# Performance work log

Measured on AMD Instinct MI355X. Metric: run time of the kernel, lower is better.

## Reference

```python
import jax, jax.numpy as jnp
import numpy as np

N_NODES = 100000


def setup_inputs() -> dict:
    key = jax.random.key(0)
    k1, k2, k3, k4 = jax.random.split(key, 4)
    N, E, D_IN, D_OUT = N_NODES, 3200000, 256, 256
    feature = jax.random.normal(k1, (N, D_IN), dtype=jnp.float32)
    edge_src = jax.random.randint(k2, (E,), 0, N, dtype=jnp.int32)
    edge_dst = jax.random.randint(k3, (E,), 0, N, dtype=jnp.int32)
    W = jax.random.normal(k4, (D_IN, D_OUT), dtype=jnp.float32) * (1.0 / np.sqrt(D_IN))
    b = jnp.zeros((D_OUT,), dtype=jnp.float32)
    return {"feature": feature, "edge_src": edge_src, "edge_dst": edge_dst, "W": W, "b": b}


def reference(feature, edge_src, edge_dst, W, b):
    # update_all(copy_src('h','m'), sum('m','h')): for each node i,
    # h_i = sum over edges (j->i) of feature[j]  -- scatter-add by destination.
    msgs = feature[edge_src]                                   # [E, D_in] (gather)
    agg = jax.ops.segment_sum(msgs, edge_dst, num_segments=N_NODES)  # [N, D_in]
    # apply_nodes: Linear + activation (relu)
    h = jnp.dot(agg, W) + b                                    # [N, D_out]
    return jax.nn.relu(h)
```

## Files before the change

### kernel.cpp

```cpp
#include <hip/hip_runtime.h>

#define D 256
#define GSIZE 16
#define TN 16
#define CSHIFT 8
#define CBIN 256
#define NCMAX 512
#define CAPC 9216
#define NB_P 256
#define TILESHIFT 12
#define NKEY 8192

using bf16x8 = __attribute__((ext_vector_type(8))) short;
using f32x4  = __attribute__((ext_vector_type(4))) float;

__device__ inline float bf_lo(unsigned int u) {
    return __builtin_bit_cast(float, u << 16);
}
__device__ inline float bf_hi(unsigned int u) {
    return __builtin_bit_cast(float, u & 0xffff0000u);
}
__device__ inline unsigned short f2bf(float f) {
    unsigned int x = __builtin_bit_cast(unsigned int, f);
    unsigned int r = (x + 0x7fffu + ((x >> 16) & 1u)) >> 16;
    return (unsigned short)r;
}

__global__ __launch_bounds__(256) void part_kernel(
    const int* __restrict__ src, const int* __restrict__ dst,
    int* __restrict__ gcntC, int* __restrict__ csrA,
    const float* __restrict__ feature, unsigned short* __restrict__ fbf, long n8,
    const float* __restrict__ W, unsigned short* __restrict__ Wt,
    int E, int NC, int chunk, int nConvF)
{
    __shared__ int h[NCMAX];
    const int b = blockIdx.x, t = threadIdx.x;

    if (b < NB_P) {
        for (int i = t; i < NC; i += 256) h[i] = 0;
        __syncthreads();
        const int beg = b * chunk;
        const int end = min(beg + chunk, E);
        for (int i = beg + t; i < end; i += 256)
            atomicAdd(&h[dst[i] >> CSHIFT], 1);
        __syncthreads();
        for (int i = t; i < NC; i += 256) {
            int c = h[i];
            h[i] = c ? atomicAdd(&gcntC[i], c) : 0;
        }
        __syncthreads();
        for (int i = beg + t; i < end; i += 256) {
            int d = dst[i];
            int c = d >> CSHIFT;
            int r = atomicAdd(&h[c], 1);
            if (r < CAPC)
                csrA[(size_t)c * CAPC + r] = (src[i] << CSHIFT) | (d & (CBIN - 1));
        }
        return;
    }
    if (b < NB_P + nConvF) {
        long i = (long)(b - NB_P) * 256 + t;
        if (i < n8) {
            const float4* p = reinterpret_cast<const float4*>(feature + i * 8);
            float4 v0 = p[0], v1 = p[1];
            uint4 r;
            r.x = (unsigned int)f2bf(v0.x) | ((unsigned int)f2bf(v0.y) << 16);
            r.y = (unsigned int)f2bf(v0.z) | ((unsigned int)f2bf(v0.w) << 16);
            r.z = (unsigned int)f2bf(v1.x) | ((unsigned int)f2bf(v1.y) << 16);
            r.w = (unsigned int)f2bf(v1.z) | ((unsigned int)f2bf(v1.w) << 16);
            *reinterpret_cast<uint4*>(fbf + i * 8) = r;
        }
        return;
    }
    int i = (b - NB_P - nConvF) * 256 + t;
    if (i < D * D / 4) {
        int n  = i >> 6;
        int k0 = (i & 63) * 4;
        float a  = W[(size_t)(k0 + 0) * D + n];
        float bb = W[(size_t)(k0 + 1) * D + n];
        float c  = W[(size_t)(k0 + 2) * D + n];
        float d  = W[(size_t)(k0 + 3) * D + n];
        uint2 r;
        r.x = (unsigned int)f2bf(a) | ((unsigned int)f2bf(bb) << 16);
        r.y = (unsigned int)f2bf(c) | ((unsigned int)f2bf(d) << 16);
        *reinterpret_cast<uint2*>(Wt + (size_t)n * D + k0) = r;
    }
}

__global__ __launch_bounds__(256) void regroup_kernel(
    const int* __restrict__ csrA, const int* __restrict__ gcntC,
    int* __restrict__ csrB, int* __restrict__ nodeBeg, int* __restrict__ nodeCnt,
    int N)
{
    __shared__ int h[NKEY];
    __shared__ int sorted[CAPC];
    __shared__ int psum[256];
    __shared__ int nBegL[CBIN], nCntL[CBIN];
    const int c = blockIdx.x, t = threadIdx.x;
    const size_t rbeg = (size_t)c * CAPC;
    const int cnt = min(gcntC[c], CAPC);

    for (int i = t; i < NKEY; i += 256) h[i] = 0;
    __syncthreads();
    for (int i = t; i < cnt; i += 256) {
        int p = csrA[rbeg + i];
        int key = ((p & (CBIN - 1)) << 5) | ((p >> CSHIFT) >> TILESHIFT);
        atomicAdd(&h[key], 1);
    }
    __syncthreads();
    int local = 0;
#pragma unroll
    for (int j = 0; j < 32; ++j) local += h[(t << 5) + j];
    psum[t] = local;
    nCntL[t] = local;
    __syncthreads();
    for (int off = 1; off < 256; off <<= 1) {
        int v = (t >= off) ? psum[t - off] : 0;
        __syncthreads();
        if (t >= off) psum[t] += v;
        __syncthreads();
    }
    int run = (t == 0) ? 0 : psum[t - 1];
    nBegL[t] = run;
#pragma unroll
    for (int j = 0; j < 32; ++j) {
        int idx = (t << 5) + j;
        int cc = h[idx];
        h[idx] = run;
        run += cc;
    }
    __syncthreads();
    for (int i = t; i < cnt; i += 256) {
        int p = csrA[rbeg + i];
        int key = ((p & (CBIN - 1)) << 5) | ((p >> CSHIFT) >> TILESHIFT);
        int r = atomicAdd(&h[key], 1);
        sorted[r] = p >> CSHIFT;
    }
    __syncthreads();
    for (int i = t; i < cnt; i += 256)
        csrB[rbeg + i] = sorted[i];
    {
        int node = (c << CSHIFT) + t;
        if (node < N) {
            nodeBeg[node] = (int)(rbeg + nBegL[t]);
            nodeCnt[node] = nCntL[t];
        }
    }
}

__global__ __launch_bounds__(256) void agg_gemm_kernel(
    const unsigned short* __restrict__ fbf,
    const int* __restrict__ csrB,
    const int* __restrict__ nodeBeg,
    const int* __restrict__ nodeCnt,
    const unsigned short* __restrict__ Wt,
    const float* __restrict__ bias,
    float* __restrict__ out, int N)
{
    __shared__ int nBeg[TN], nCnt[TN];
    __shared__ unsigned short A[TN][D + 8];

    const int blk  = blockIdx.x;
    const int t    = threadIdx.x;
    const int wave = t >> 6;
    const int lane = t & 63;
    const int sub  = lane & 31;
    const int half = lane >> 5;
    const int node0 = blk * TN;
    const size_t colOff = (size_t)(sub << 3);

    if (t < TN) {
        int node = node0 + t;
        nBeg[t] = (node < N) ? nodeBeg[node] : 0;
        nCnt[t] = (node < N) ? nodeCnt[node] : 0;
    }
    __syncthreads();

    for (int ni = 0; ni < 4; ++ni) {
        const int l = (wave << 2) + ni;
        const int node = node0 + l;
        float a0 = 0.f, a1 = 0.f, a2 = 0.f, a3 = 0.f;
        float a4 = 0.f, a5 = 0.f, a6 = 0.f, a7 = 0.f;
        if (node < N) {
            const int b0 = nBeg[l];
            const int c0 = nCnt[l];
            int j = 0;
            for (; j + 3 < c0; j += 4) {
                int s0 = csrB[b0 + j + half];
                int s1 = csrB[b0 + j + 2 + half];
                uint4 v0 = *reinterpret_cast<const uint4*>(fbf + ((size_t)s0 << 8) + colOff);
                uint4 v1 = *reinterpret_cast<const uint4*>(fbf + ((size_t)s1 << 8) + colOff);
                a0 += bf_lo(v0.x); a1 += bf_hi(v0.x); a2 += bf_lo(v0.y); a3 += bf_hi(v0.y);
                a4 += bf_lo(v0.z); a5 += bf_hi(v0.z); a6 += bf_lo(v0.w); a7 += bf_hi(v0.w);
                a0 += bf_lo(v1.x); a1 += bf_hi(v1.x); a2 += bf_lo(v1.y); a3 += bf_hi(v1.y);
                a4 += bf_lo(v1.z); a5 += bf_hi(v1.z); a6 += bf_lo(v1.w); a7 += bf_hi(v1.w);
            }
            if (j + 1 < c0) {
                int s0 = csrB[b0 + j + half];
                uint4 v0 = *reinterpret_cast<const uint4*>(fbf + ((size_t)s0 << 8) + colOff);
                a0 += bf_lo(v0.x); a1 += bf_hi(v0.x); a2 += bf_lo(v0.y); a3 += bf_hi(v0.y);
                a4 += bf_lo(v0.z); a5 += bf_hi(v0.z); a6 += bf_lo(v0.w); a7 += bf_hi(v0.w);
                j += 2;
            }
            if (j < c0 && half == 0) {
                int s0 = csrB[b0 + j];
                uint4 v0 = *reinterpret_cast<const uint4*>(fbf + ((size_t)s0 << 8) + colOff);
                a0 += bf_lo(v0.x); a1 += bf_hi(v0.x); a2 += bf_lo(v0.y); a3 += bf_hi(v0.y);
                a4 += bf_lo(v0.z); a5 += bf_hi(v0.z); a6 += bf_lo(v0.w); a7 += bf_hi(v0.w);
            }
        }
        a0 += __shfl_xor(a0, 32); a1 += __shfl_xor(a1, 32);
        a2 += __shfl_xor(a2, 32); a3 += __shfl_xor(a3, 32);
        a4 += __shfl_xor(a4, 32); a5 += __shfl_xor(a5, 32);
        a6 += __shfl_xor(a6, 32); a7 += __shfl_xor(a7, 32);
        if (half == 0) {
            uint4 r;
            r.x = (unsigned int)f2bf(a0) | ((unsigned int)f2bf(a1) << 16);
            r.y = (unsigned int)f2bf(a2) | ((unsigned int)f2bf(a3) << 16);
            r.z = (unsigned int)f2bf(a4) | ((unsigned int)f2bf(a5) << 16);
            r.w = (unsigned int)f2bf(a6) | ((unsigned int)f2bf(a7) << 16);
            *reinterpret_cast<uint4*>(&A[l][sub << 3]) = r;
        }
    }
    __syncthreads();

    const int lr = lane & 15;
    const int lg = lane >> 4;

    bf16x8 afr[8];
#pragma unroll
    for (int ks = 0; ks < 8; ++ks)
        afr[ks] = *reinterpret_cast<const bf16x8*>(&A[lr][ks * 32 + lg * 8]);

#pragma unroll
    for (int c = 0; c < 4; ++c) {
        const int ct = (wave << 2) + c;
        f32x4 acc = {0.f, 0.f, 0.f, 0.f};
        const unsigned short* bp = Wt + (size_t)(ct * 16 + lr) * D + lg * 8;
#pragma unroll
        for (int ks = 0; ks < 8; ++ks) {
            bf16x8 bfr = *reinterpret_cast<const bf16x8*>(bp + ks * 32);
            acc = __builtin_amdgcn_mfma_f32_16x16x32_bf16(afr[ks], bfr, acc, 0, 0, 0);
        }
        const float bv = bias[ct * 16 + lr];
#pragma unroll
        for (int jj = 0; jj < 4; ++jj) {
            int row = node0 + lg * 4 + jj;
            if (row < N) {
                float v = acc[jj] + bv;
                out[(size_t)row * D + ct * 16 + lr] = v > 0.f ? v : 0.f;
            }
        }
    }
}

__global__ __launch_bounds__(256) void scatter_kernel(
    const float* __restrict__ feature, const int* __restrict__ src,
    const int* __restrict__ dst, float* __restrict__ agg, int E)
{
    int edge = blockIdx.x * (blockDim.x >> 6) + (threadIdx.x >> 6);
    int lane = threadIdx.x & 63;
    if (edge >= E) return;
    int s = src[edge];
    int d = dst[edge];
    const float4 v = *reinterpret_cast<const float4*>(feature + (size_t)s * D + lane * 4);
    float* o = agg + (size_t)d * D + lane * 4;
    atomicAdd(o + 0, v.x);
    atomicAdd(o + 1, v.y);
    atomicAdd(o + 2, v.z);
    atomicAdd(o + 3, v.w);
}

#define BM 32
__global__ __launch_bounds__(256) void linear_relu_kernel(
    float* __restrict__ h, const float* __restrict__ W,
    const float* __restrict__ b, int n_nodes)
{
    __shared__ float sA[BM][D];
    const int node0 = blockIdx.x * BM;
    const int t = threadIdx.x;
    for (int m = 0; m < BM; ++m) {
        int nd = node0 + m;
        sA[m][t] = (nd < n_nodes) ? h[(size_t)nd * D + t] : 0.0f;
    }
    __syncthreads();
    float acc[BM];
#pragma unroll
    for (int m = 0; m < BM; ++m) acc[m] = 0.0f;
    for (int kk = 0; kk < D; ++kk) {
        float w = W[kk * D + t];
#pragma unroll
        for (int m = 0; m < BM; ++m) acc[m] += sA[m][kk] * w;
    }
    const float bias = b[t];
    for (int m = 0; m < BM; ++m) {
        int nd = node0 + m;
        if (nd < n_nodes) {
            float v = acc[m] + bias;
            h[(size_t)nd * D + t] = v > 0.0f ? v : 0.0f;
        }
    }
}

extern "C" void kernel_launch(void* const* d_in, const int* in_sizes, int n_in,
                              void* d_out, int out_size, void* d_ws, size_t ws_size,
                              hipStream_t stream)
{
    const float* feature = (const float*)d_in[0];
    const int*   src     = (const int*)d_in[1];
    const int*   dst     = (const int*)d_in[2];
    const float* W       = (const float*)d_in[3];
    const float* b       = (const float*)d_in[4];
    float*       out     = (float*)d_out;

    const int E = in_sizes[1];
    const int N = in_sizes[0] / D;
    const int NC = (N + CBIN - 1) >> CSHIFT;
    const int chunk = (E + NB_P - 1) / NB_P;

    size_t off = 0;
    auto alloc = [&](size_t bytes, size_t align) {
        off = (off + align - 1) / align * align;
        size_t r = off; off += bytes; return r;
    };
    size_t o_gcntC = alloc((size_t)NC * 4, 16);
    size_t o_csrA  = alloc((size_t)NC * CAPC * 4, 16);
    size_t o_csrB  = alloc((size_t)NC * CAPC * 4, 16);
    size_t o_nbeg  = alloc((size_t)N * 4, 16);
    size_t o_ncnt  = alloc((size_t)N * 4, 16);
    size_t o_wt    = alloc((size_t)D * D * 2, 16);
    size_t o_fbf   = alloc((size_t)N * D * 2, 16);
    size_t need_full = off;

    char* ws = (char*)d_ws;

    const double mc = (double)E / NC;
    const bool cap_ok =
        (mc + 8.0 * __builtin_sqrt(mc) + 16.0 <= (double)CAPC) &&
        (NC <= NCMAX) &&
        (N <= (32 << TILESHIFT));

    if (ws_size >= need_full && cap_ok) {
        int* gcntC   = (int*)(ws + o_gcntC);
        int* csrA    = (int*)(ws + o_csrA);
        int* csrB    = (int*)(ws + o_csrB);
        int* nodeBeg = (int*)(ws + o_nbeg);
        int* nodeCnt = (int*)(ws + o_ncnt);
        unsigned short* Wt  = (unsigned short*)(ws + o_wt);
        unsigned short* fbf = (unsigned short*)(ws + o_fbf);

        const long n8 = (long)N * D / 8;
        const int nConvF = (int)((n8 + 255) / 256);
        const int nConvW = (D * D / 4 + 255) / 256;

        hipMemsetAsync(gcntC, 0, (size_t)NC * 4, stream);

        part_kernel<<<NB_P + nConvF + nConvW, 256, 0, stream>>>(
            src, dst, gcntC, csrA, feature, fbf, n8, W, Wt,
            E, NC, chunk, nConvF);

        regroup_kernel<<<NC, 256, 0, stream>>>(
            csrA, gcntC, csrB, nodeBeg, nodeCnt, N);

        agg_gemm_kernel<<<(N + TN - 1) / TN, 256, 0, stream>>>(
            fbf, csrB, nodeBeg, nodeCnt, Wt, b, out, N);
    } else {
        hipMemsetAsync(d_out, 0, (size_t)out_size * sizeof(float), stream);
        scatter_kernel<<<(E + 3) / 4, 256, 0, stream>>>(feature, src, dst, out, E);
        linear_relu_kernel<<<(N + BM - 1) / BM, 256, 0, stream>>>(out, W, b, N);
    }
}
```

Baseline: 425.2 us.

## Drop source-tile sub-sort in regroup and stage per-block edge lists in LDS

The regroup kernel no longer sub-sorts each destination's edges by source tile. It now does a plain 256-bin counting sort by destination, with a smaller histogram and fewer passes. The aggregation kernel copies the contiguous edge-index range for its 16 destination nodes into shared memory, falling back to global memory if the range exceeds 1536 entries. It then gathers from LDS instead of issuing scattered global index loads. Losing the source-tile ordering may reduce L2 locality of the feature gathers, which could offset the cheaper regroup.

```diff
diff --git a/kernel.cpp b/kernel.cpp
--- a/kernel.cpp
+++ b/kernel.cpp
@@ -1,15 +1,13 @@
 #include <hip/hip_runtime.h>
 
 #define D 256
-#define GSIZE 16
 #define TN 16
 #define CSHIFT 8
 #define CBIN 256
 #define NCMAX 512
 #define CAPC 9216
 #define NB_P 256
-#define TILESHIFT 12
-#define NKEY 8192
+#define CAPL 1536
 
 using bf16x8 = __attribute__((ext_vector_type(8))) short;
 using f32x4  = __attribute__((ext_vector_type(4))) float;
@@ -92,27 +90,19 @@
     int* __restrict__ csrB, int* __restrict__ nodeBeg, int* __restrict__ nodeCnt,
     int N)
 {
-    __shared__ int h[NKEY];
+    __shared__ int h[CBIN], psum[CBIN], cur[CBIN];
     __shared__ int sorted[CAPC];
-    __shared__ int psum[256];
-    __shared__ int nBegL[CBIN], nCntL[CBIN];
     const int c = blockIdx.x, t = threadIdx.x;
-    const size_t rbeg = (size_t)c * CAPC;
+    const int rbeg = c * CAPC;
     const int cnt = min(gcntC[c], CAPC);
 
-    for (int i = t; i < NKEY; i += 256) h[i] = 0;
-    __syncthreads();
-    for (int i = t; i < cnt; i += 256) {
-        int p = csrA[rbeg + i];
-        int key = ((p & (CBIN - 1)) << 5) | ((p >> CSHIFT) >> TILESHIFT);
-        atomicAdd(&h[key], 1);
-    }
-    __syncthreads();
-    int local = 0;
-#pragma unroll
-    for (int j = 0; j < 32; ++j) local += h[(t << 5) + j];
-    psum[t] = local;
-    nCntL[t] = local;
+    h[t] = 0;
+    __syncthreads();
+    for (int i = t; i < cnt; i += 256)
+        atomicAdd(&h[csrA[(size_t)rbeg + i] & (CBIN - 1)], 1);
+    __syncthreads();
+    const int myCnt = h[t];
+    psum[t] = myCnt;
     __syncthreads();
     for (int off = 1; off < 256; off <<= 1) {
         int v = (t >= off) ? psum[t - off] : 0;
@@ -120,32 +110,24 @@
         if (t >= off) psum[t] += v;
         __syncthreads();
     }
-    int run = (t == 0) ? 0 : psum[t - 1];
-    nBegL[t] = run;
-#pragma unroll
-    for (int j = 0; j < 32; ++j) {
-        int idx = (t << 5) + j;
-        int cc = h[idx];
-        h[idx] = run;
-        run += cc;
-    }
-    __syncthreads();
-    for (int i = t; i < cnt; i += 256) {
-        int p = csrA[rbeg + i];
-        int key = ((p & (CBIN - 1)) << 5) | ((p >> CSHIFT) >> TILESHIFT);
-        int r = atomicAdd(&h[key], 1);
-        sorted[r] = p >> CSHIFT;
-    }
-    __syncthreads();
-    for (int i = t; i < cnt; i += 256)
-        csrB[rbeg + i] = sorted[i];
+    const int excl = psum[t] - myCnt;
+    cur[t] = excl;
     {
         int node = (c << CSHIFT) + t;
         if (node < N) {
-            nodeBeg[node] = (int)(rbeg + nBegL[t]);
-            nodeCnt[node] = nCntL[t];
-        }
-    }
+            nodeBeg[node] = rbeg + excl;
+            nodeCnt[node] = myCnt;
+        }
+    }
+    __syncthreads();
+    for (int i = t; i < cnt; i += 256) {
+        int p = csrA[(size_t)rbeg + i];
+        int r = atomicAdd(&cur[p & (CBIN - 1)], 1);
+        sorted[r] = p >> CSHIFT;
+    }
+    __syncthreads();
+    for (int i = t; i < cnt; i += 256)
+        csrB[(size_t)rbeg + i] = sorted[i];
 }
 
 __global__ __launch_bounds__(256) void agg_gemm_kernel(
@@ -157,7 +139,9 @@
     const float* __restrict__ bias,
     float* __restrict__ out, int N)
 {
-    __shared__ int nBeg[TN], nCnt[TN];
+    __shared__ int lsrc[CAPL];
+    __shared__ int lBeg[TN], lCnt[TN];
+    __shared__ int sB, sL, sFit;
     __shared__ unsigned short A[TN][D + 8];
 
     const int blk  = blockIdx.x;
@@ -171,8 +155,22 @@
 
     if (t < TN) {
         int node = node0 + t;
-        nBeg[t] = (node < N) ? nodeBeg[node] : 0;
-        nCnt[t] = (node < N) ? nodeCnt[node] : 0;
+        bool valid = node < N;
+        lBeg[t] = valid ? nodeBeg[node] : 0;
+        lCnt[t] = valid ? nodeCnt[node] : 0;
+    }
+    __syncthreads();
+    if (t == 0) {
+        int lastL = min(TN - 1, N - 1 - node0);
+        sB = lBeg[0];
+        sL = lBeg[lastL] + lCnt[lastL] - lBeg[0];
+        sFit = (sL <= CAPL);
+    }
+    __syncthreads();
+    const int segB = sB, segL = sL, fit = sFit;
+    if (fit) {
+        for (int i = t; i < segL; i += 256)
+            lsrc[i] = csrB[(size_t)segB + i];
     }
     __syncthreads();
 
@@ -182,12 +180,13 @@
         float a0 = 0.f, a1 = 0.f, a2 = 0.f, a3 = 0.f;
         float a4 = 0.f, a5 = 0.f, a6 = 0.f, a7 = 0.f;
         if (node < N) {
-            const int b0 = nBeg[l];
-            const int c0 = nCnt[l];
+            const int* elist = fit ? lsrc : (csrB + segB);
+            const int b0 = lBeg[l] - segB;
+            const int c0 = lCnt[l];
             int j = 0;
             for (; j + 3 < c0; j += 4) {
-                int s0 = csrB[b0 + j + half];
-                int s1 = csrB[b0 + j + 2 + half];
+                int s0 = elist[b0 + j + half];
+                int s1 = elist[b0 + j + 2 + half];
                 uint4 v0 = *reinterpret_cast<const uint4*>(fbf + ((size_t)s0 << 8) + colOff);
                 uint4 v1 = *reinterpret_cast<const uint4*>(fbf + ((size_t)s1 << 8) + colOff);
                 a0 += bf_lo(v0.x); a1 += bf_hi(v0.x); a2 += bf_lo(v0.y); a3 += bf_hi(v0.y);
@@ -196,14 +195,14 @@
                 a4 += bf_lo(v1.z); a5 += bf_hi(v1.z); a6 += bf_lo(v1.w); a7 += bf_hi(v1.w);
             }
             if (j + 1 < c0) {
-                int s0 = csrB[b0 + j + half];
+                int s0 = elist[b0 + j + half];
                 uint4 v0 = *reinterpret_cast<const uint4*>(fbf + ((size_t)s0 << 8) + colOff);
                 a0 += bf_lo(v0.x); a1 += bf_hi(v0.x); a2 += bf_lo(v0.y); a3 += bf_hi(v0.y);
                 a4 += bf_lo(v0.z); a5 += bf_hi(v0.z); a6 += bf_lo(v0.w); a7 += bf_hi(v0.w);
                 j += 2;
             }
             if (j < c0 && half == 0) {
-                int s0 = csrB[b0 + j];
+                int s0 = elist[b0 + j];
                 uint4 v0 = *reinterpret_cast<const uint4*>(fbf + ((size_t)s0 << 8) + colOff);
                 a0 += bf_lo(v0.x); a1 += bf_hi(v0.x); a2 += bf_lo(v0.y); a3 += bf_hi(v0.y);
                 a4 += bf_lo(v0.z); a5 += bf_hi(v0.z); a6 += bf_lo(v0.w); a7 += bf_hi(v0.w);
@@ -337,8 +336,7 @@
     const double mc = (double)E / NC;
     const bool cap_ok =
         (mc + 8.0 * __builtin_sqrt(mc) + 16.0 <= (double)CAPC) &&
-        (NC <= NCMAX) &&
-        (N <= (32 << TILESHIFT));
+        (NC <= NCMAX);
 
     if (ws_size >= need_full && cap_ok) {
         int* gcntC   = (int*)(ws + o_gcntC);
```

After: 404.6 us. 4.8% less time.
